# Kernel optimization log

Hardware: AMD Instinct MI355X
Metric: run time of the kernel (lower is better)

Reference implementation:

```python
import jax, jax.numpy as jnp
import numpy as np

H = 2            # attention heads
HID = 128        # hidden_channels
NEG_SLOPE = 0.2  # GATConv leaky_relu slope

N_USER, N_POST, N_ENT = 100000, 50000, 20000
TEXT_D, USER_D, ENT_D = 768, 64, 64
E_PUB, E_REP, E_CON, E_INT, E_FOL = 150000, 300000, 200000, 500000, 500000


def _gat(h_src, h_dst, src, dst, Wsrc, Wdst, asrc, adst, bias):
    """PyG GATConv((-1,-1), C, heads=H, concat=False, add_self_loops=False)."""
    n_dst = h_dst.shape[0]
    C = Wsrc.shape[1] // H
    xs = (h_src @ Wsrc).reshape(-1, H, C)          # [Ns,H,C]
    xd = (h_dst @ Wdst).reshape(-1, H, C)          # [Nd,H,C]
    al_s = jnp.einsum('nhc,hc->nh', xs, asrc)      # [Ns,H]
    al_d = jnp.einsum('nhc,hc->nh', xd, adst)      # [Nd,H]
    e = jax.nn.leaky_relu(al_s[src] + al_d[dst], NEG_SLOPE)   # [E,H]
    m = jax.ops.segment_max(e, dst, num_segments=n_dst)
    m = jnp.where(jnp.isfinite(m), m, 0.0)
    ex = jnp.exp(e - m[dst])
    denom = jax.ops.segment_sum(ex, dst, num_segments=n_dst)
    alpha = ex / (denom[dst] + 1e-16)              # per-dst softmax
    msg = xs[src] * alpha[:, :, None]              # [E,H,C]
    out = jax.ops.segment_sum(msg, dst, num_segments=n_dst)   # [Nd,H,C]
    return out.mean(axis=1) + bias                 # concat=False -> head mean


def setup_inputs() -> dict:
    key = jax.random.key(0)
    ks = jax.random.split(key, 24)
    s = 0.05
    d = {
        'post_cls': jax.random.normal(ks[0], (N_POST, TEXT_D), jnp.float32),
        'user_x': jax.random.normal(ks[1], (N_USER, USER_D), jnp.float32),
        'entity_x': jax.random.normal(ks[2], (N_ENT, ENT_D), jnp.float32),
        'Wpost': jax.random.normal(ks[3], (TEXT_D, HID), jnp.float32) * s,
        'bpost': jnp.zeros((HID,), jnp.float32),
        'Wuser': jax.random.normal(ks[4], (USER_D, HID), jnp.float32) * s,
        'buser': jnp.zeros((HID,), jnp.float32),
        'Went': jax.random.normal(ks[5], (ENT_D, HID), jnp.float32) * s,
        'bent': jnp.zeros((HID,), jnp.float32),
        # 2 layers x 5 relations (publish, repost, contain, interact, follow)
        'gat_Wsrc': jax.random.normal(ks[6], (2, 5, HID, H * HID), jnp.float32) * s,
        'gat_Wdst': jax.random.normal(ks[7], (2, 5, HID, H * HID), jnp.float32) * s,
        'gat_asrc': jax.random.normal(ks[8], (2, 5, H, HID), jnp.float32) * s,
        'gat_adst': jax.random.normal(ks[9], (2, 5, H, HID), jnp.float32) * s,
        'gat_bias': jnp.zeros((2, 5, HID), jnp.float32),
        'Wc1': jax.random.normal(ks[10], (HID, HID // 2), jnp.float32) * s,
        'bc1': jnp.zeros((HID // 2,), jnp.float32),
        'Wc2': jax.random.normal(ks[11], (HID // 2, 1), jnp.float32) * s,
        'bc2': jnp.zeros((1,), jnp.float32),
        'pub_src': jax.random.randint(ks[12], (E_PUB,), 0, N_USER, jnp.int32),
        'pub_dst': jax.random.randint(ks[13], (E_PUB,), 0, N_POST, jnp.int32),
        'rep_src': jax.random.randint(ks[14], (E_REP,), 0, N_USER, jnp.int32),
        'rep_dst': jax.random.randint(ks[15], (E_REP,), 0, N_POST, jnp.int32),
        'con_src': jax.random.randint(ks[16], (E_CON,), 0, N_POST, jnp.int32),
        'con_dst': jax.random.randint(ks[17], (E_CON,), 0, N_ENT, jnp.int32),
        'int_src': jax.random.randint(ks[18], (E_INT,), 0, N_USER, jnp.int32),
        'int_dst': jax.random.randint(ks[19], (E_INT,), 0, N_USER, jnp.int32),
        'fol_src': jax.random.randint(ks[20], (E_FOL,), 0, N_USER, jnp.int32),
        'fol_dst': jax.random.randint(ks[21], (E_FOL,), 0, N_USER, jnp.int32),
    }
    return d


def _forward(post_cls, user_x, entity_x, Wpost, bpost, Wuser, buser, Went, bent,
             gat_Wsrc, gat_Wdst, gat_asrc, gat_adst, gat_bias,
             Wc1, bc1, Wc2, bc2, edges):
    h = {
        'post': post_cls @ Wpost + bpost,
        'user': user_x @ Wuser + buser,
        'entity': entity_x @ Went + bent,
    }
    for l in range(2):
        def g(r, h_src, h_dst, src, dst):
            return _gat(h_src, h_dst, src, dst,
                        gat_Wsrc[l, r], gat_Wdst[l, r],
                        gat_asrc[l, r], gat_adst[l, r], gat_bias[l, r])
        # HeteroConv aggr='sum' over edge types sharing a dst node type
        new_post = (g(0, h['user'], h['post'], edges['pub_src'], edges['pub_dst'])
                    + g(1, h['user'], h['post'], edges['rep_src'], edges['rep_dst']))
        new_ent = g(2, h['post'], h['entity'], edges['con_src'], edges['con_dst'])
        new_user = (g(3, h['user'], h['user'], edges['int_src'], edges['int_dst'])
                    + g(4, h['user'], h['user'], edges['fol_src'], edges['fol_dst']))
        h = {'post': jax.nn.relu(new_post),
             'user': jax.nn.relu(new_user),
             'entity': jax.nn.relu(new_ent)}
    # classifier (dropout inactive at inference)
    z = jax.nn.relu(h['post'] @ Wc1 + bc1)
    out = z @ Wc2 + bc2
    return out.squeeze(-1)   # [n_posts]


def reference(post_cls, user_x, entity_x, Wpost, bpost, Wuser, buser, Went, bent,
              gat_Wsrc, gat_Wdst, gat_asrc, gat_adst, gat_bias,
              Wc1, bc1, Wc2, bc2,
              pub_src, pub_dst, rep_src, rep_dst, con_src, con_dst,
              int_src, int_dst, fol_src, fol_dst):
    edges = dict(pub_src=pub_src, pub_dst=pub_dst, rep_src=rep_src, rep_dst=rep_dst,
                 con_src=con_src, con_dst=con_dst, int_src=int_src, int_dst=int_dst,
                 fol_src=fol_src, fol_dst=fol_dst)
    return _forward(post_cls, user_x, entity_x, Wpost, bpost, Wuser, buser, Went, bent,
                    gat_Wsrc, gat_Wdst, gat_asrc, gat_adst, gat_bias,
                    Wc1, bc1, Wc2, bc2, edges)
```

## Files before the change

kernel.cpp:

```cpp
#include <hip/hip_runtime.h>
#include <cstdint>
#include <cstddef>

#define N_USER 100000
#define N_POST 50000
#define TEXT_D 768
#define USER_D 64
#define E_TOT 1450000
#define N_TOT 300000

typedef unsigned short ushort_t;
typedef float f4v __attribute__((ext_vector_type(4)));
typedef short s8v __attribute__((ext_vector_type(8)));
typedef unsigned short u4v __attribute__((ext_vector_type(4)));
typedef unsigned short u8v __attribute__((ext_vector_type(8)));

__device__ __forceinline__ float leaky(float v) { return v > 0.f ? v : 0.2f * v; }
__device__ __forceinline__ void split_bf(float x, ushort_t& hi, ushort_t& lo) {
  unsigned u = __float_as_uint(x);
  hi = (ushort_t)(u >> 16);
  float r = x - __uint_as_float(u & 0xFFFF0000u);
  lo = (ushort_t)(__float_as_uint(r) >> 16);
}

struct Ptrs4 { const int* p[4]; };

__global__ void wvec_kernel(const float* __restrict__ W, const float* __restrict__ av,
                            float* __restrict__ wv) {
  int b = blockIdx.x;
  int lr = b / 2, h = b % 2;
  const float* Wp = W + ((size_t)lr * 128 * 256) + (size_t)threadIdx.x * 256 + h * 128;
  const float* ap = av + (size_t)(lr * 2 + h) * 128;
  float acc = 0.f;
  for (int c = 0; c < 128; ++c) acc += Wp[c] * ap[c];
  wv[(size_t)(lr * 2 + h) * 128 + threadIdx.x] = acc;
}

__global__ void wt_prep(const float* __restrict__ W, ushort_t* __restrict__ WTh,
                        ushort_t* __restrict__ WTl, int K, int C) {
  int k = blockIdx.x * 256 + threadIdx.x;
  int c = blockIdx.y;
  if (k >= K) return;
  ushort_t h, l;
  split_bf(W[(size_t)k * C + c], h, l);
  WTh[(size_t)c * K + k] = h;
  WTl[(size_t)c * K + k] = l;
}

__global__ void stk_prep(const float* __restrict__ Wa, const float* __restrict__ Wb,
                         ushort_t* __restrict__ STh, ushort_t* __restrict__ STl) {
  int rel = blockIdx.x;
  int c = blockIdx.y;
  int t = threadIdx.x;
  const float* W = rel ? Wb : Wa;
  float v = W[(size_t)(t & 127) * 256 + (size_t)(t >> 7) * 128 + c];
  ushort_t hh, ll;
  split_bf(v, hh, ll);
  size_t idx = (size_t)c * 512 + (size_t)rel * 256 + t;
  STh[idx] = hh;
  STl[idx] = ll;
}

__global__ void bias_sum(const float* __restrict__ gbias, float* __restrict__ BS) {
  int c = threadIdx.x;
  BS[c]       = gbias[0 * 640 + 0 * 128 + c] + gbias[0 * 640 + 1 * 128 + c];
  BS[128 + c] = gbias[0 * 640 + 3 * 128 + c] + gbias[0 * 640 + 4 * 128 + c];
  BS[256 + c] = gbias[1 * 640 + 0 * 128 + c] + gbias[1 * 640 + 1 * 128 + c];
}

template <bool ASPLIT, bool RELU>
__global__ __launch_bounds__(512) void gemm_bregs(const void* __restrict__ Ag,
                                                  const ushort_t* __restrict__ Agl,
                                                  const ushort_t* __restrict__ Bgh,
                                                  const ushort_t* __restrict__ Bgl,
                                                  const float* __restrict__ bv,
                                                  float* __restrict__ Out,
                                                  int N, int K) {
  __shared__ ushort_t LAh[64 * 72], LAl[64 * 72];
  int t = threadIdx.x;
  int lane = t & 63, w = t >> 6;
  int m = lane & 15, quad = lane >> 4;
  int row0 = blockIdx.x * 64;
  int nkc = K >> 6;

  const float* Xf = (const float*)Ag;
  const ushort_t* Xh = (const ushort_t*)Ag;

  int sr = t >> 3, sk = (t & 7) * 8;
  int srow = row0 + sr; if (srow >= N) srow = N - 1;
  size_t abase = (size_t)srow * K + sk;

  size_t bb = (size_t)(w * 16 + m) * K;

  f4v acc[4];
#pragma unroll
  for (int mt = 0; mt < 4; ++mt) acc[mt] = (f4v){0.f, 0.f, 0.f, 0.f};

  float4 pf0, pf1;
  u8v ph, pl;
  auto LOADA = [&](int kc) {
    size_t off = abase + (size_t)kc * 64;
    if constexpr (ASPLIT) {
      ph = *(const u8v*)(Xh + off);
      pl = *(const u8v*)(Agl + off);
    } else {
      pf0 = *(const float4*)(Xf + off);
      pf1 = *(const float4*)(Xf + off + 4);
    }
  };
  auto WRITEA = [&]() {
    if constexpr (ASPLIT) {
      *(u8v*)&LAh[sr * 72 + sk] = ph;
      *(u8v*)&LAl[sr * 72 + sk] = pl;
    } else {
      u8v hh, ll;
      ushort_t h_, l_;
      split_bf(pf0.x, h_, l_); hh[0] = h_; ll[0] = l_;
      split_bf(pf0.y, h_, l_); hh[1] = h_; ll[1] = l_;
      split_bf(pf0.z, h_, l_); hh[2] = h_; ll[2] = l_;
      split_bf(pf0.w, h_, l_); hh[3] = h_; ll[3] = l_;
      split_bf(pf1.x, h_, l_); hh[4] = h_; ll[4] = l_;
      split_bf(pf1.y, h_, l_); hh[5] = h_; ll[5] = l_;
      split_bf(pf1.z, h_, l_); hh[6] = h_; ll[6] = l_;
      split_bf(pf1.w, h_, l_); hh[7] = h_; ll[7] = l_;
      *(u8v*)&LAh[sr * 72 + sk] = hh;
      *(u8v*)&LAl[sr * 72 + sk] = ll;
    }
  };

  LOADA(0);
  for (int kc = 0; kc < nkc; ++kc) {
    WRITEA();
    __syncthreads();
    if (kc + 1 < nkc) LOADA(kc + 1);
    size_t bo = bb + (size_t)kc * 64 + quad * 8;
    s8v bh0 = *(const s8v*)(Bgh + bo);
    s8v bl0 = *(const s8v*)(Bgl + bo);
    s8v bh1 = *(const s8v*)(Bgh + bo + 32);
    s8v bl1 = *(const s8v*)(Bgl + bo + 32);
#pragma unroll
    for (int mt = 0; mt < 4; ++mt) {
      int ar = (mt * 16 + m) * 72 + quad * 8;
      s8v ah = *(const s8v*)&LAh[ar];
      s8v al = *(const s8v*)&LAl[ar];
      acc[mt] = __builtin_amdgcn_mfma_f32_16x16x32_bf16(ah, bh0, acc[mt], 0, 0, 0);
      acc[mt] = __builtin_amdgcn_mfma_f32_16x16x32_bf16(ah, bl0, acc[mt], 0, 0, 0);
      acc[mt] = __builtin_amdgcn_mfma_f32_16x16x32_bf16(al, bh0, acc[mt], 0, 0, 0);
    }
#pragma unroll
    for (int mt = 0; mt < 4; ++mt) {
      int ar = (mt * 16 + m) * 72 + 32 + quad * 8;
      s8v ah = *(const s8v*)&LAh[ar];
      s8v al = *(const s8v*)&LAl[ar];
      acc[mt] = __builtin_amdgcn_mfma_f32_16x16x32_bf16(ah, bh1, acc[mt], 0, 0, 0);
      acc[mt] = __builtin_amdgcn_mfma_f32_16x16x32_bf16(ah, bl1, acc[mt], 0, 0, 0);
      acc[mt] = __builtin_amdgcn_mfma_f32_16x16x32_bf16(al, bh1, acc[mt], 0, 0, 0);
    }
    __syncthreads();
  }

  float bbv = bv[w * 16 + m];
#pragma unroll
  for (int mt = 0; mt < 4; ++mt)
#pragma unroll
    for (int j = 0; j < 4; ++j) {
      int row = row0 + mt * 16 + quad * 4 + j;
      if (row < N) {
        float vv = acc[mt][j] + bbv;
        if (RELU) vv = fmaxf(vv, 0.f);
        Out[(size_t)row * 128 + w * 16 + m] = vv;
      }
    }
}

__device__ __forceinline__ void rel_of(int g, int& r, int& loc, int& nb) {
  if (g < 450000) {
    if (g < 150000) { r = 0; loc = g;          nb = 0; }
    else            { r = 1; loc = g - 150000; nb = 50000; }
  } else if (g < 950000)  { r = 2; loc = g - 450000;  nb = 100000; }
  else                    { r = 3; loc = g - 950000;  nb = 200000; }
}
__global__ void histc_kernel(Ptrs4 dsts, int* __restrict__ cnt) {
  int g = blockIdx.x * 256 + threadIdx.x;
  if (g >= E_TOT) return;
  int r, loc, nb;
  rel_of(g, r, loc, nb);
  atomicAdd(&cnt[nb + dsts.p[r][loc]], 1);
}
__global__ __launch_bounds__(256) void scan1_kernel(const int* __restrict__ cnt,
                                                    int* __restrict__ excl,
                                                    int* __restrict__ partials, int Nd) {
  __shared__ int sb[256];
  int t = threadIdx.x;
  int base = blockIdx.x * 1024 + t * 4;
  int v[4];
#pragma unroll
  for (int j = 0; j < 4; ++j) v[j] = (base + j < Nd) ? cnt[base + j] : 0;
  int tot = v[0] + v[1] + v[2] + v[3];
  sb[t] = tot;
  __syncthreads();
  for (int off = 1; off < 256; off <<= 1) {
    int x = 0;
    if (t >= off) x = sb[t - off];
    __syncthreads();
    sb[t] += x;
    __syncthreads();
  }
  int ex = sb[t] - tot;
  if (t == 255) partials[blockIdx.x] = sb[t];
  int run = ex;
#pragma unroll
  for (int j = 0; j < 4; ++j) {
    if (base + j < Nd) excl[base + j] = run;
    run += v[j];
  }
}
__global__ __launch_bounds__(512) void scan2_kernel(int* __restrict__ partials, int B) {
  __shared__ int sb[512];
  int t = threadIdx.x;
  int v = (t < B) ? partials[t] : 0;
  sb[t] = v;
  __syncthreads();
  for (int off = 1; off < 512; off <<= 1) {
    int x = 0;
    if (t >= off) x = sb[t - off];
    __syncthreads();
    sb[t] += x;
    __syncthreads();
  }
  if (t < B) partials[t] = sb[t] - v;
}
__global__ void scan3_kernel(const int* __restrict__ excl, const int* __restrict__ partials,
                             int* __restrict__ rowptr, int* __restrict__ cursor) {
  int i = blockIdx.x * 256 + threadIdx.x;
  if (i < N_TOT) {
    int v = excl[i] + partials[i >> 10];
    rowptr[i] = v;
    cursor[i] = v;
  }
  if (i == 0) rowptr[N_TOT] = E_TOT;
}
__global__ void scatterc_kernel(Ptrs4 srcs, Ptrs4 dsts,
                                int* __restrict__ cursor, int* __restrict__ csrc) {
  int g = blockIdx.x * 256 + threadIdx.x;
  if (g >= E_TOT) return;
  int r, loc, nb;
  rel_of(g, r, loc, nb);
  int p = atomicAdd(&cursor[nb + dsts.p[r][loc]], 1);
  csrc[p] = srcs.p[r][loc];
}

__global__ __launch_bounds__(256) void logits2_kernel(const float* __restrict__ H,
                                                      const float* __restrict__ wsA,
                                                      const float* __restrict__ wsB,
                                                      float* __restrict__ alsA,
                                                      float* __restrict__ alsB, int Ns) {
  int n = blockIdx.x * 4 + (threadIdx.x >> 6);
  int lane = threadIdx.x & 63;
  if (n >= Ns) return;
  const float* hr = H + (size_t)n * 128;
  float ha = hr[lane], hb = hr[lane + 64];
  float p0 = ha * wsA[lane] + hb * wsA[lane + 64];
  float p1 = ha * wsA[128 + lane] + hb * wsA[192 + lane];
  float p2 = ha * wsB[lane] + hb * wsB[lane + 64];
  float p3 = ha * wsB[128 + lane] + hb * wsB[192 + lane];
#pragma unroll
  for (int mk = 32; mk; mk >>= 1) {
    p0 += __shfl_xor(p0, mk); p1 += __shfl_xor(p1, mk);
    p2 += __shfl_xor(p2, mk); p3 += __shfl_xor(p3, mk);
  }
  if (lane == 0) {
    *(float2*)(alsA + 2 * (size_t)n) = make_float2(p0, p1);
    *(float2*)(alsB + 2 * (size_t)n) = make_float2(p2, p3);
  }
}

__global__ __launch_bounds__(256) void aggG2_kernel(const int* __restrict__ rowA,
                                                    const int* __restrict__ rowB,
                                                    const int* __restrict__ csrc,
                                                    const float* __restrict__ alsA,
                                                    const float* __restrict__ alsB,
                                                    const float* __restrict__ wdvA,
                                                    const float* __restrict__ wdvB,
                                                    const float* __restrict__ Hs,
                                                    const float* __restrict__ Hd,
                                                    ushort_t* __restrict__ Gh,
                                                    ushort_t* __restrict__ Gl,
                                                    int Nd, int dOff) {
  int w = threadIdx.x >> 6;
  int lane = threadIdx.x & 63;
  int rel = w & 1;
  int hw = lane >> 5, s = lane & 31;
  int dl = blockIdx.x * 4 + (w >> 1) * 2 + hw;
  if (dl >= Nd) return;
  int d = dl + dOff;
  const int* rp = rel ? rowB : rowA;
  const float* als = rel ? alsB : alsA;
  const float* wdv = rel ? wdvB : wdvA;

  const float* hr = Hd + (size_t)d * 128;
  float t0 = 0.f, t1 = 0.f;
#pragma unroll
  for (int j = 0; j < 4; ++j) {
    float hv = hr[s + 32 * j];
    t0 += hv * wdv[s + 32 * j];
    t1 += hv * wdv[128 + s + 32 * j];
  }
#pragma unroll
  for (int mk = 16; mk; mk >>= 1) { t0 += __shfl_xor(t0, mk); t1 += __shfl_xor(t1, mk); }

  int start = rp[d], end = rp[d + 1];
  float den0 = 0.f, den1 = 0.f;
  f4v a0 = (f4v){0.f, 0.f, 0.f, 0.f}, a1 = (f4v){0.f, 0.f, 0.f, 0.f};
  if (end > start) {
    int last = end - 1;
    for (int b0 = start; b0 < end; b0 += 8) {
      int sid[8]; bool vl[8];
#pragma unroll
      for (int j = 0; j < 8; ++j) {
        int ee = b0 + j;
        vl[j] = ee < end;
        sid[j] = csrc[vl[j] ? ee : last];
      }
      float2 al[8]; f4v x[8];
#pragma unroll
      for (int j = 0; j < 8; ++j) {
        al[j] = *(const float2*)(als + 2 * (size_t)sid[j]);
        x[j] = *(const f4v*)(Hs + (size_t)sid[j] * 128 + 4 * s);
      }
#pragma unroll
      for (int j = 0; j < 8; ++j) {
        float w0 = vl[j] ? __expf(leaky(al[j].x + t0)) : 0.f;
        float w1 = vl[j] ? __expf(leaky(al[j].y + t1)) : 0.f;
        den0 += w0; den1 += w1;
#pragma unroll
        for (int q = 0; q < 4; ++q) { a0[q] += w0 * x[j][q]; a1[q] += w1 * x[j][q]; }
      }
    }
  }
  float i0 = 0.5f / (den0 + 1e-16f);
  float i1 = 0.5f / (den1 + 1e-16f);
  ushort_t* gh = Gh + (size_t)dl * 512 + rel * 256;
  ushort_t* gl = Gl + (size_t)dl * 512 + rel * 256;
  u4v g0h, g0l, g1h, g1l;
#pragma unroll
  for (int q = 0; q < 4; ++q) {
    ushort_t hh, ll;
    split_bf(a0[q] * i0, hh, ll); g0h[q] = hh; g0l[q] = ll;
    split_bf(a1[q] * i1, hh, ll); g1h[q] = hh; g1l[q] = ll;
  }
  *(u4v*)(gh + 4 * s) = g0h;
  *(u4v*)(gl + 4 * s) = g0l;
  *(u4v*)(gh + 128 + 4 * s) = g1h;
  *(u4v*)(gl + 128 + 4 * s) = g1l;
}

__global__ __launch_bounds__(256) void classifier_kernel(const float* __restrict__ Hp,
                                                         const float* __restrict__ Wc1, const float* __restrict__ bc1,
                                                         const float* __restrict__ Wc2, const float* __restrict__ bc2,
                                                         float* __restrict__ out, int N) {
  __shared__ float sW[128 * 64];
  int t = threadIdx.x;
#pragma unroll
  for (int i = 0; i < 8; ++i) ((float4*)sW)[t + 256 * i] = ((const float4*)Wc1)[t + 256 * i];
  __syncthreads();
  int lane = t & 63, wv = t >> 6;
  float b = bc1[lane], w2 = Wc2[lane], b2 = bc2[0];
#pragma unroll
  for (int nn = 0; nn < 2; ++nn) {
    int n = blockIdx.x * 8 + wv * 2 + nn;
    if (n >= N) continue;
    const float* hr = Hp + (size_t)n * 128;
    float accz = b;
    for (int k = 0; k < 128; ++k) accz += hr[k] * sW[k * 64 + lane];
    float z = fmaxf(accz, 0.f) * w2;
#pragma unroll
    for (int off = 32; off; off >>= 1) z += __shfl_down(z, off);
    if (lane == 0) out[n] = z + b2;
  }
}

extern "C" void kernel_launch(void* const* d_in, const int* in_sizes, int n_in,
                              void* d_out, int out_size, void* d_ws, size_t ws_size,
                              hipStream_t stream) {
  const float* post_cls = (const float*)d_in[0];
  const float* user_x   = (const float*)d_in[1];
  const float* Wpost = (const float*)d_in[3];
  const float* bpost = (const float*)d_in[4];
  const float* Wuser = (const float*)d_in[5];
  const float* buser = (const float*)d_in[6];
  const float* gWsrc = (const float*)d_in[9];
  const float* gWdst = (const float*)d_in[10];
  const float* gasrc = (const float*)d_in[11];
  const float* gadst = (const float*)d_in[12];
  const float* gbias = (const float*)d_in[13];
  const float* Wc1 = (const float*)d_in[14];
  const float* bc1 = (const float*)d_in[15];
  const float* Wc2 = (const float*)d_in[16];
  const float* bc2 = (const float*)d_in[17];
  Ptrs4 SRCS, DSTS;
  SRCS.p[0] = (const int*)d_in[18]; DSTS.p[0] = (const int*)d_in[19];
  SRCS.p[1] = (const int*)d_in[20]; DSTS.p[1] = (const int*)d_in[21];
  SRCS.p[2] = (const int*)d_in[24]; DSTS.p[2] = (const int*)d_in[25];
  SRCS.p[3] = (const int*)d_in[26]; DSTS.p[3] = (const int*)d_in[27];
  float* out = (float*)d_out;
  (void)ws_size; (void)in_sizes; (void)n_in; (void)out_size;

  float* Wf = (float*)d_ws;
  size_t o = 0;
  float* WDSTV = Wf + o; o += 2560;
  float* WSRCV = Wf + o; o += 2560;
  float* BS    = Wf + o; o += 384;
  float* ALSa  = Wf + o; o += (size_t)N_USER * 2;
  float* ALSb  = Wf + o; o += (size_t)N_USER * 2;
  float* HU    = Wf + o; o += (size_t)N_USER * 128;
  float* HP    = Wf + o; o += (size_t)N_POST * 128;
  float* TMP   = Wf + o; o += (size_t)N_POST * 128;
  int* Wi = (int*)(Wf + o);
  size_t io = 0;
  int* RP   = Wi + io; io += N_TOT + 1;
  int* CURS = Wi + io; io += N_TOT;
  int* CNT  = Wi + io; io += N_TOT;
  int* EXCL = Wi + io; io += N_TOT;
  int* PART = Wi + io; io += 512;
  int* CSRC = Wi + io; io += E_TOT;
  io = (io + 7) & ~(size_t)7;
  ushort_t* Wu = (ushort_t*)(Wi + io);
  size_t uo = 0;
  ushort_t* PWh = Wu + uo; uo += 128 * TEXT_D;
  ushort_t* PWl = Wu + uo; uo += 128 * TEXT_D;
  ushort_t* UWh = Wu + uo; uo += 128 * USER_D;
  ushort_t* UWl = Wu + uo; uo += 128 * USER_D;
  ushort_t* STh[3]; ushort_t* STl[3];
  for (int i = 0; i < 3; ++i) {
    STh[i] = Wu + uo; uo += 128 * 512;
    STl[i] = Wu + uo; uo += 128 * 512;
  }
  ushort_t* Gh = Wu + uo; uo += (size_t)N_POST * 512;
  ushort_t* Gl = Wu + uo; uo += (size_t)N_POST * 512;

  const int NOFF_PUB = 0, NOFF_REP = 50000, NOFF_INT = 100000, NOFF_FOL = 200000;

  (void)hipMemsetAsync(CNT, 0, (size_t)N_TOT * sizeof(int), stream);
  histc_kernel<<<(E_TOT + 255) / 256, 256, 0, stream>>>(DSTS, CNT);
  int B = (N_TOT + 1023) / 1024;
  scan1_kernel<<<B, 256, 0, stream>>>(CNT, EXCL, PART, N_TOT);
  scan2_kernel<<<1, 512, 0, stream>>>(PART, B);
  scan3_kernel<<<(N_TOT + 255) / 256, 256, 0, stream>>>(EXCL, PART, RP, CURS);
  scatterc_kernel<<<(E_TOT + 255) / 256, 256, 0, stream>>>(SRCS, DSTS, CURS, CSRC);

  wt_prep<<<dim3(3, 128), 256, 0, stream>>>(Wpost, PWh, PWl, TEXT_D, 128);
  wt_prep<<<dim3(1, 128), 256, 0, stream>>>(Wuser, UWh, UWl, USER_D, 128);
  stk_prep<<<dim3(2, 128), 256, 0, stream>>>(gWsrc + (size_t)0 * 32768, gWsrc + (size_t)1 * 32768, STh[0], STl[0]);
  stk_prep<<<dim3(2, 128), 256, 0, stream>>>(gWsrc + (size_t)3 * 32768, gWsrc + (size_t)4 * 32768, STh[1], STl[1]);
  stk_prep<<<dim3(2, 128), 256, 0, stream>>>(gWsrc + (size_t)5 * 32768, gWsrc + (size_t)6 * 32768, STh[2], STl[2]);
  wvec_kernel<<<20, 128, 0, stream>>>(gWdst, gadst, WDSTV);
  wvec_kernel<<<20, 128, 0, stream>>>(gWsrc, gasrc, WSRCV);
  bias_sum<<<1, 128, 0, stream>>>(gbias, BS);

  gemm_bregs<false, false><<<(N_POST + 63) / 64, 512, 0, stream>>>(
      post_cls, nullptr, PWh, PWl, bpost, HP, N_POST, TEXT_D);
  gemm_bregs<false, false><<<(N_USER + 63) / 64, 512, 0, stream>>>(
      user_x, nullptr, UWh, UWl, buser, HU, N_USER, USER_D);

  logits2_kernel<<<(N_USER + 3) / 4, 256, 0, stream>>>(
      HU, WSRCV + 0 * 256, WSRCV + 1 * 256, ALSa, ALSb, N_USER);
  aggG2_kernel<<<(N_POST + 3) / 4, 256, 0, stream>>>(
      RP + NOFF_PUB, RP + NOFF_REP, CSRC, ALSa, ALSb,
      WDSTV + 0 * 256, WDSTV + 1 * 256, HU, HP, Gh, Gl, N_POST, 0);
  gemm_bregs<true, true><<<(N_POST + 63) / 64, 512, 0, stream>>>(
      Gh, Gl, STh[0], STl[0], BS + 0, HP, N_POST, 512);

  logits2_kernel<<<(N_USER + 3) / 4, 256, 0, stream>>>(
      HU, WSRCV + 3 * 256, WSRCV + 4 * 256, ALSa, ALSb, N_USER);
  aggG2_kernel<<<(50000 + 3) / 4, 256, 0, stream>>>(
      RP + NOFF_INT, RP + NOFF_FOL, CSRC, ALSa, ALSb,
      WDSTV + 3 * 256, WDSTV + 4 * 256, HU, HU, Gh, Gl, 50000, 0);
  gemm_bregs<true, true><<<(50000 + 63) / 64, 512, 0, stream>>>(
      Gh, Gl, STh[1], STl[1], BS + 128, TMP, 50000, 512);
  aggG2_kernel<<<(50000 + 3) / 4, 256, 0, stream>>>(
      RP + NOFF_INT, RP + NOFF_FOL, CSRC, ALSa, ALSb,
      WDSTV + 3 * 256, WDSTV + 4 * 256, HU, HU, Gh, Gl, 50000, 50000);
  gemm_bregs<true, true><<<(50000 + 63) / 64, 512, 0, stream>>>(
      Gh, Gl, STh[1], STl[1], BS + 128, HU + (size_t)50000 * 128, 50000, 512);
  (void)hipMemcpyAsync(HU, TMP, (size_t)50000 * 128 * sizeof(float),
                       hipMemcpyDeviceToDevice, stream);

  logits2_kernel<<<(N_USER + 3) / 4, 256, 0, stream>>>(
      HU, WSRCV + 5 * 256, WSRCV + 6 * 256, ALSa, ALSb, N_USER);
  aggG2_kernel<<<(N_POST + 3) / 4, 256, 0, stream>>>(
      RP + NOFF_PUB, RP + NOFF_REP, CSRC, ALSa, ALSb,
      WDSTV + 5 * 256, WDSTV + 6 * 256, HU, HP, Gh, Gl, N_POST, 0);
  gemm_bregs<true, true><<<(N_POST + 63) / 64, 512, 0, stream>>>(
      Gh, Gl, STh[2], STl[2], BS + 256, HP, N_POST, 512);

  classifier_kernel<<<(N_POST + 7) / 8, 256, 0, stream>>>(HP, Wc1, bc1, Wc2, bc2, out, N_POST);
}
```

Before: 1.127 ms.

## Fuse GAT neighbor aggregation with stacked projection GEMM per 16-node tile

```diff
diff --git a/kernel.cpp b/kernel.cpp
--- a/kernel.cpp
+++ b/kernel.cpp
@@ -68,9 +68,7 @@
   BS[256 + c] = gbias[1 * 640 + 0 * 128 + c] + gbias[1 * 640 + 1 * 128 + c];
 }
 
-template <bool ASPLIT, bool RELU>
-__global__ __launch_bounds__(512) void gemm_bregs(const void* __restrict__ Ag,
-                                                  const ushort_t* __restrict__ Agl,
+__global__ __launch_bounds__(512) void gemm_bregs(const float* __restrict__ Xf,
                                                   const ushort_t* __restrict__ Bgh,
                                                   const ushort_t* __restrict__ Bgl,
                                                   const float* __restrict__ bv,
@@ -83,13 +81,9 @@
   int row0 = blockIdx.x * 64;
   int nkc = K >> 6;
 
-  const float* Xf = (const float*)Ag;
-  const ushort_t* Xh = (const ushort_t*)Ag;
-
   int sr = t >> 3, sk = (t & 7) * 8;
   int srow = row0 + sr; if (srow >= N) srow = N - 1;
   size_t abase = (size_t)srow * K + sk;
-
   size_t bb = (size_t)(w * 16 + m) * K;
 
   f4v acc[4];
@@ -97,35 +91,24 @@
   for (int mt = 0; mt < 4; ++mt) acc[mt] = (f4v){0.f, 0.f, 0.f, 0.f};
 
   float4 pf0, pf1;
-  u8v ph, pl;
   auto LOADA = [&](int kc) {
     size_t off = abase + (size_t)kc * 64;
-    if constexpr (ASPLIT) {
-      ph = *(const u8v*)(Xh + off);
-      pl = *(const u8v*)(Agl + off);
-    } else {
-      pf0 = *(const float4*)(Xf + off);
-      pf1 = *(const float4*)(Xf + off + 4);
-    }
+    pf0 = *(const float4*)(Xf + off);
+    pf1 = *(const float4*)(Xf + off + 4);
   };
   auto WRITEA = [&]() {
-    if constexpr (ASPLIT) {
-      *(u8v*)&LAh[sr * 72 + sk] = ph;
-      *(u8v*)&LAl[sr * 72 + sk] = pl;
-    } else {
-      u8v hh, ll;
-      ushort_t h_, l_;
-      split_bf(pf0.x, h_, l_); hh[0] = h_; ll[0] = l_;
-      split_bf(pf0.y, h_, l_); hh[1] = h_; ll[1] = l_;
-      split_bf(pf0.z, h_, l_); hh[2] = h_; ll[2] = l_;
-      split_bf(pf0.w, h_, l_); hh[3] = h_; ll[3] = l_;
-      split_bf(pf1.x, h_, l_); hh[4] = h_; ll[4] = l_;
-      split_bf(pf1.y, h_, l_); hh[5] = h_; ll[5] = l_;
-      split_bf(pf1.z, h_, l_); hh[6] = h_; ll[6] = l_;
-      split_bf(pf1.w, h_, l_); hh[7] = h_; ll[7] = l_;
-      *(u8v*)&LAh[sr * 72 + sk] = hh;
-      *(u8v*)&LAl[sr * 72 + sk] = ll;
-    }
+    u8v hh, ll;
+    ushort_t h_, l_;
+    split_bf(pf0.x, h_, l_); hh[0] = h_; ll[0] = l_;
+    split_bf(pf0.y, h_, l_); hh[1] = h_; ll[1] = l_;
+    split_bf(pf0.z, h_, l_); hh[2] = h_; ll[2] = l_;
+    split_bf(pf0.w, h_, l_); hh[3] = h_; ll[3] = l_;
+    split_bf(pf1.x, h_, l_); hh[4] = h_; ll[4] = l_;
+    split_bf(pf1.y, h_, l_); hh[5] = h_; ll[5] = l_;
+    split_bf(pf1.z, h_, l_); hh[6] = h_; ll[6] = l_;
+    split_bf(pf1.w, h_, l_); hh[7] = h_; ll[7] = l_;
+    *(u8v*)&LAh[sr * 72 + sk] = hh;
+    *(u8v*)&LAl[sr * 72 + sk] = ll;
   };
 
   LOADA(0);
@@ -165,11 +148,7 @@
 #pragma unroll
     for (int j = 0; j < 4; ++j) {
       int row = row0 + mt * 16 + quad * 4 + j;
-      if (row < N) {
-        float vv = acc[mt][j] + bbv;
-        if (RELU) vv = fmaxf(vv, 0.f);
-        Out[(size_t)row * 128 + w * 16 + m] = vv;
-      }
+      if (row < N) Out[(size_t)row * 128 + w * 16 + m] = acc[mt][j] + bbv;
     }
 }
 
@@ -275,84 +254,121 @@
   }
 }
 
-__global__ __launch_bounds__(256) void aggG2_kernel(const int* __restrict__ rowA,
-                                                    const int* __restrict__ rowB,
-                                                    const int* __restrict__ csrc,
-                                                    const float* __restrict__ alsA,
-                                                    const float* __restrict__ alsB,
-                                                    const float* __restrict__ wdvA,
-                                                    const float* __restrict__ wdvB,
-                                                    const float* __restrict__ Hs,
-                                                    const float* __restrict__ Hd,
-                                                    ushort_t* __restrict__ Gh,
-                                                    ushort_t* __restrict__ Gl,
-                                                    int Nd, int dOff) {
-  int w = threadIdx.x >> 6;
-  int lane = threadIdx.x & 63;
-  int rel = w & 1;
-  int hw = lane >> 5, s = lane & 31;
-  int dl = blockIdx.x * 4 + (w >> 1) * 2 + hw;
-  if (dl >= Nd) return;
-  int d = dl + dOff;
-  const int* rp = rel ? rowB : rowA;
-  const float* als = rel ? alsB : alsA;
-  const float* wdv = rel ? wdvB : wdvA;
-
-  const float* hr = Hd + (size_t)d * 128;
-  float t0 = 0.f, t1 = 0.f;
-#pragma unroll
-  for (int j = 0; j < 4; ++j) {
-    float hv = hr[s + 32 * j];
-    t0 += hv * wdv[s + 32 * j];
-    t1 += hv * wdv[128 + s + 32 * j];
-  }
-#pragma unroll
-  for (int mk = 16; mk; mk >>= 1) { t0 += __shfl_xor(t0, mk); t1 += __shfl_xor(t1, mk); }
-
-  int start = rp[d], end = rp[d + 1];
-  float den0 = 0.f, den1 = 0.f;
-  f4v a0 = (f4v){0.f, 0.f, 0.f, 0.f}, a1 = (f4v){0.f, 0.f, 0.f, 0.f};
-  if (end > start) {
-    int last = end - 1;
-    for (int b0 = start; b0 < end; b0 += 8) {
-      int sid[8]; bool vl[8];
-#pragma unroll
-      for (int j = 0; j < 8; ++j) {
-        int ee = b0 + j;
-        vl[j] = ee < end;
-        sid[j] = csrc[vl[j] ? ee : last];
-      }
-      float2 al[8]; f4v x[8];
-#pragma unroll
-      for (int j = 0; j < 8; ++j) {
-        al[j] = *(const float2*)(als + 2 * (size_t)sid[j]);
-        x[j] = *(const f4v*)(Hs + (size_t)sid[j] * 128 + 4 * s);
-      }
-#pragma unroll
-      for (int j = 0; j < 8; ++j) {
-        float w0 = vl[j] ? __expf(leaky(al[j].x + t0)) : 0.f;
-        float w1 = vl[j] ? __expf(leaky(al[j].y + t1)) : 0.f;
-        den0 += w0; den1 += w1;
-#pragma unroll
-        for (int q = 0; q < 4; ++q) { a0[q] += w0 * x[j][q]; a1[q] += w1 * x[j][q]; }
+__global__ __launch_bounds__(256) void fusedagg_kernel(const int* __restrict__ rowA,
+                                                       const int* __restrict__ rowB,
+                                                       const int* __restrict__ csrc,
+                                                       const float* __restrict__ alsA,
+                                                       const float* __restrict__ alsB,
+                                                       const float* __restrict__ wdvA,
+                                                       const float* __restrict__ wdvB,
+                                                       const float* __restrict__ Hs,
+                                                       const float* __restrict__ Hd,
+                                                       const ushort_t* __restrict__ Bgh,
+                                                       const ushort_t* __restrict__ Bgl,
+                                                       const float* __restrict__ bsv,
+                                                       float* __restrict__ Out, int Nd) {
+  __shared__ ushort_t LGh[16 * 544], LGl[16 * 544];
+  int t = threadIdx.x;
+  int hw = t >> 5;
+  int s = t & 31;
+  int d0 = blockIdx.x * 16;
+
+#pragma unroll 1
+  for (int i = 0; i < 4; ++i) {
+    int tid = hw * 4 + i;
+    int dl = tid >> 1, rel = tid & 1;
+    int d = d0 + dl;
+    const int* rp = rel ? rowB : rowA;
+    const float* als = rel ? alsB : alsA;
+    const float* wdv = rel ? wdvB : wdvA;
+
+    const float* hr = Hd + (size_t)d * 128;
+    float t0 = 0.f, t1 = 0.f;
+#pragma unroll
+    for (int j = 0; j < 4; ++j) {
+      float hv = hr[s + 32 * j];
+      t0 += hv * wdv[s + 32 * j];
+      t1 += hv * wdv[128 + s + 32 * j];
+    }
+#pragma unroll
+    for (int mk = 16; mk; mk >>= 1) { t0 += __shfl_xor(t0, mk); t1 += __shfl_xor(t1, mk); }
+
+    int start = rp[d], end = rp[d + 1];
+    float den0 = 0.f, den1 = 0.f;
+    f4v a0 = (f4v){0.f, 0.f, 0.f, 0.f}, a1 = (f4v){0.f, 0.f, 0.f, 0.f};
+    if (end > start) {
+      int last = end - 1;
+      for (int b0 = start; b0 < end; b0 += 8) {
+        int sid[8]; bool vl[8];
+#pragma unroll
+        for (int j = 0; j < 8; ++j) {
+          int ee = b0 + j;
+          vl[j] = ee < end;
+          sid[j] = csrc[vl[j] ? ee : last];
+        }
+        float2 al2[8]; f4v x[8];
+#pragma unroll
+        for (int j = 0; j < 8; ++j) {
+          al2[j] = *(const float2*)(als + 2 * (size_t)sid[j]);
+          x[j] = *(const f4v*)(Hs + (size_t)sid[j] * 128 + 4 * s);
+        }
+#pragma unroll
+        for (int j = 0; j < 8; ++j) {
+          float w0 = vl[j] ? __expf(leaky(al2[j].x + t0)) : 0.f;
+          float w1 = vl[j] ? __expf(leaky(al2[j].y + t1)) : 0.f;
+          den0 += w0; den1 += w1;
+#pragma unroll
+          for (int q = 0; q < 4; ++q) { a0[q] += w0 * x[j][q]; a1[q] += w1 * x[j][q]; }
+        }
       }
     }
-  }
-  float i0 = 0.5f / (den0 + 1e-16f);
-  float i1 = 0.5f / (den1 + 1e-16f);
-  ushort_t* gh = Gh + (size_t)dl * 512 + rel * 256;
-  ushort_t* gl = Gl + (size_t)dl * 512 + rel * 256;
-  u4v g0h, g0l, g1h, g1l;
-#pragma unroll
-  for (int q = 0; q < 4; ++q) {
-    ushort_t hh, ll;
-    split_bf(a0[q] * i0, hh, ll); g0h[q] = hh; g0l[q] = ll;
-    split_bf(a1[q] * i1, hh, ll); g1h[q] = hh; g1l[q] = ll;
-  }
-  *(u4v*)(gh + 4 * s) = g0h;
-  *(u4v*)(gl + 4 * s) = g0l;
-  *(u4v*)(gh + 128 + 4 * s) = g1h;
-  *(u4v*)(gl + 128 + 4 * s) = g1l;
+    float i0 = 0.5f / (den0 + 1e-16f);
+    float i1 = 0.5f / (den1 + 1e-16f);
+    int base = dl * 544 + rel * 256;
+    u4v g0h, g0l, g1h, g1l;
+#pragma unroll
+    for (int q = 0; q < 4; ++q) {
+      ushort_t hh, ll;
+      split_bf(a0[q] * i0, hh, ll); g0h[q] = hh; g0l[q] = ll;
+      split_bf(a1[q] * i1, hh, ll); g1h[q] = hh; g1l[q] = ll;
+    }
+    *(u4v*)&LGh[base + 4 * s] = g0h;
+    *(u4v*)&LGl[base + 4 * s] = g0l;
+    *(u4v*)&LGh[base + 128 + 4 * s] = g1h;
+    *(u4v*)&LGl[base + 128 + 4 * s] = g1l;
+  }
+  __syncthreads();
+
+  int lane = t & 63, w = t >> 6;
+  int m = lane & 15, quad = lane >> 4;
+  f4v acc0 = (f4v){0.f, 0.f, 0.f, 0.f};
+  f4v acc1 = (f4v){0.f, 0.f, 0.f, 0.f};
+  size_t cb0 = (size_t)(w * 32 + m) * 512;
+  size_t cb1 = (size_t)(w * 32 + 16 + m) * 512;
+#pragma unroll
+  for (int kc = 0; kc < 16; ++kc) {
+    int ko = kc * 32 + quad * 8;
+    s8v ah = *(const s8v*)&LGh[m * 544 + ko];
+    s8v al = *(const s8v*)&LGl[m * 544 + ko];
+    s8v b0h = *(const s8v*)(Bgh + cb0 + ko);
+    s8v b0l = *(const s8v*)(Bgl + cb0 + ko);
+    s8v b1h = *(const s8v*)(Bgh + cb1 + ko);
+    s8v b1l = *(const s8v*)(Bgl + cb1 + ko);
+    acc0 = __builtin_amdgcn_mfma_f32_16x16x32_bf16(ah, b0h, acc0, 0, 0, 0);
+    acc0 = __builtin_amdgcn_mfma_f32_16x16x32_bf16(ah, b0l, acc0, 0, 0, 0);
+    acc0 = __builtin_amdgcn_mfma_f32_16x16x32_bf16(al, b0h, acc0, 0, 0, 0);
+    acc1 = __builtin_amdgcn_mfma_f32_16x16x32_bf16(ah, b1h, acc1, 0, 0, 0);
+    acc1 = __builtin_amdgcn_mfma_f32_16x16x32_bf16(ah, b1l, acc1, 0, 0, 0);
+    acc1 = __builtin_amdgcn_mfma_f32_16x16x32_bf16(al, b1h, acc1, 0, 0, 0);
+  }
+  float bb0 = bsv[w * 32 + m], bb1 = bsv[w * 32 + 16 + m];
+#pragma unroll
+  for (int j = 0; j < 4; ++j) {
+    int row = d0 + quad * 4 + j;
+    float* o = Out + (size_t)row * 128 + w * 32;
+    o[m] = fmaxf(acc0[j] + bb0, 0.f);
+    o[16 + m] = fmaxf(acc1[j] + bb1, 0.f);
+  }
 }
 
 __global__ __launch_bounds__(256) void classifier_kernel(const float* __restrict__ Hp,
@@ -414,8 +430,8 @@
   float* ALSa  = Wf + o; o += (size_t)N_USER * 2;
   float* ALSb  = Wf + o; o += (size_t)N_USER * 2;
   float* HU    = Wf + o; o += (size_t)N_USER * 128;
+  float* HU2   = Wf + o; o += (size_t)N_USER * 128;
   float* HP    = Wf + o; o += (size_t)N_POST * 128;
-  float* TMP   = Wf + o; o += (size_t)N_POST * 128;
   int* Wi = (int*)(Wf + o);
   size_t io = 0;
   int* RP   = Wi + io; io += N_TOT + 1;
@@ -436,8 +452,6 @@
     STh[i] = Wu + uo; uo += 128 * 512;
     STl[i] = Wu + uo; uo += 128 * 512;
   }
-  ushort_t* Gh = Wu + uo; uo += (size_t)N_POST * 512;
-  ushort_t* Gl = Wu + uo; uo += (size_t)N_POST * 512;
 
   const int NOFF_PUB = 0, NOFF_REP = 50000, NOFF_INT = 100000, NOFF_FOL = 200000;
 
@@ -458,41 +472,31 @@
   wvec_kernel<<<20, 128, 0, stream>>>(gWsrc, gasrc, WSRCV);
   bias_sum<<<1, 128, 0, stream>>>(gbias, BS);
 
-  gemm_bregs<false, false><<<(N_POST + 63) / 64, 512, 0, stream>>>(
-      post_cls, nullptr, PWh, PWl, bpost, HP, N_POST, TEXT_D);
-  gemm_bregs<false, false><<<(N_USER + 63) / 64, 512, 0, stream>>>(
-      user_x, nullptr, UWh, UWl, buser, HU, N_USER, USER_D);
+  gemm_bregs<<<(N_POST + 63) / 64, 512, 0, stream>>>(
+      post_cls, PWh, PWl, bpost, HP, N_POST, TEXT_D);
+  gemm_bregs<<<(N_USER + 63) / 64, 512, 0, stream>>>(
+      user_x, UWh, UWl, buser, HU, N_USER, USER_D);
 
   logits2_kernel<<<(N_USER + 3) / 4, 256, 0, stream>>>(
       HU, WSRCV + 0 * 256, WSRCV + 1 * 256, ALSa, ALSb, N_USER);
-  aggG2_kernel<<<(N_POST + 3) / 4, 256, 0, stream>>>(
+  fusedagg_kernel<<<N_POST / 16, 256, 0, stream>>>(
       RP + NOFF_PUB, RP + NOFF_REP, CSRC, ALSa, ALSb,
-      WDSTV + 0 * 256, WDSTV + 1 * 256, HU, HP, Gh, Gl, N_POST, 0);
-  gemm_bregs<true, true><<<(N_POST + 63) / 64, 512, 0, stream>>>(
-      Gh, Gl, STh[0], STl[0], BS + 0, HP, N_POST, 512);
+      WDSTV + 0 * 256, WDSTV + 1 * 256, HU, HP,
+      STh[0], STl[0], BS + 0, HP, N_POST);
 
   logits2_kernel<<<(N_USER + 3) / 4, 256, 0, stream>>>(
       HU, WSRCV + 3 * 256, WSRCV + 4 * 256, ALSa, ALSb, N_USER);
-  aggG2_kernel<<<(50000 + 3) / 4, 256, 0, stream>>>(
+  fusedagg_kernel<<<N_USER / 16, 256, 0, stream>>>(
       RP + NOFF_INT, RP + NOFF_FOL, CSRC, ALSa, ALSb,
-      WDSTV + 3 * 256, WDSTV + 4 * 256, HU, HU, Gh, Gl, 50000, 0);
-  gemm_bregs<true, true><<<(50000 + 63) / 64, 512, 0, stream>>>(
-      Gh, Gl, STh[1], STl[1], BS + 128, TMP, 50000, 512);
-  aggG2_kernel<<<(50000 + 3) / 4, 256, 0, stream>>>(
-      RP + NOFF_INT, RP + NOFF_FOL, CSRC, ALSa, ALSb,
-      WDSTV + 3 * 256, WDSTV + 4 * 256, HU, HU, Gh, Gl, 50000, 50000);
-  gemm_bregs<true, true><<<(50000 + 63) / 64, 512, 0, stream>>>(
-      Gh, Gl, STh[1], STl[1], BS + 128, HU + (size_t)50000 * 128, 50000, 512);
-  (void)hipMemcpyAsync(HU, TMP, (size_t)50000 * 128 * sizeof(float),
-                       hipMemcpyDeviceToDevice, stream);
+      WDSTV + 3 * 256, WDSTV + 4 * 256, HU, HU,
+      STh[1], STl[1], BS + 128, HU2, N_USER);
 
   logits2_kernel<<<(N_USER + 3) / 4, 256, 0, stream>>>(
-      HU, WSRCV + 5 * 256, WSRCV + 6 * 256, ALSa, ALSb, N_USER);
-  aggG2_kernel<<<(N_POST + 3) / 4, 256, 0, stream>>>(
+      HU2, WSRCV + 5 * 256, WSRCV + 6 * 256, ALSa, ALSb, N_USER);
+  fusedagg_kernel<<<N_POST / 16, 256, 0, stream>>>(
       RP + NOFF_PUB, RP + NOFF_REP, CSRC, ALSa, ALSb,
-      WDSTV + 5 * 256, WDSTV + 6 * 256, HU, HP, Gh, Gl, N_POST, 0);
-  gemm_bregs<true, true><<<(N_POST + 63) / 64, 512, 0, stream>>>(
-      Gh, Gl, STh[2], STl[2], BS + 256, HP, N_POST, 512);
+      WDSTV + 5 * 256, WDSTV + 6 * 256, HU2, HP,
+      STh[2], STl[2], BS + 256, HP, N_POST);
 
   classifier_kernel<<<(N_POST + 7) / 8, 256, 0, stream>>>(HP, Wc1, bc1, Wc2, bc2, out, N_POST);
 }
```

Result: slower. 1.203 ms (+6.8%).
